# Kernel tuning notes

Measured on AMD Instinct MI355X. Metric: run time of the kernel, lower is better.

Reference implementation:

```python
import jax, jax.numpy as jnp
import numpy as np

HIDDEN_DIM = 2048
N = 4  # expansion_rate
LAYER_IDX = 0
S_ALPHA = 0.01
S_BETA = 0.01
EPS = 1e-5


def setup_inputs() -> dict:
    key = jax.random.key(0)
    k1, k2, k3, k4, k5 = jax.random.split(key, 5)
    batch, seq = 4, 2048
    layer_output = jax.random.normal(k1, (batch, seq, HIDDEN_DIM), dtype=jnp.float32)
    hidden_states = jax.random.normal(k2, (batch, seq, N, HIDDEN_DIM), dtype=jnp.float32)
    # static base matrices (initialization from the torch module)
    B = jnp.ones((1, N), dtype=jnp.float32)
    Am = jnp.zeros((N, 1), dtype=jnp.float32).at[LAYER_IDX % N, 0].set(1.0)
    Ar = jnp.eye(N, dtype=jnp.float32)
    # dynamic parameters
    s_alpha = jnp.full((N, N), S_ALPHA, dtype=jnp.float32)
    s_beta = jnp.full((1, N), S_BETA, dtype=jnp.float32)
    W_beta = jax.random.normal(k3, (HIDDEN_DIM, N), dtype=jnp.float32) * 0.02
    W_m = jax.random.normal(k4, (HIDDEN_DIM, N), dtype=jnp.float32) * 0.02
    W_r = jax.random.normal(k5, (HIDDEN_DIM, N, N), dtype=jnp.float32) * 0.02
    return {
        "layer_output": layer_output,
        "hidden_states": hidden_states,
        "B": B,
        "Am": Am,
        "Ar": Ar,
        "s_alpha": s_alpha,
        "s_beta": s_beta,
        "W_beta": W_beta,
        "W_m": W_m,
        "W_r": W_r,
    }


def reference(layer_output, hidden_states, B, Am, Ar, s_alpha, s_beta, W_beta, W_m, W_r):
    # hidden_states: [b, s, n, d]; layer_output: [b, s, d]
    # --- dynamic matrices ---
    mu = jnp.mean(hidden_states, axis=-1, keepdims=True)
    var = jnp.var(hidden_states, axis=-1, keepdims=True)
    H_norm = (hidden_states - mu) * jax.lax.rsqrt(var + EPS)  # layer_norm, no affine
    H_bar = H_norm.mean(axis=2)  # [b, s, d]

    delta_B = jnp.tanh(H_bar @ W_beta)            # [b, s, n]
    B_dyn = s_beta[0] * delta_B + B[0]            # [b, s, n]
    delta_Am = jnp.tanh(H_bar @ W_m)              # [b, s, n]
    Am_dyn = s_alpha[:, 0] * delta_Am + Am[:, 0]  # [b, s, n]
    delta_Ar = jnp.tanh(jnp.einsum('bsd,dij->bsij', H_bar, W_r))  # [b, s, n, n]
    Ar_dyn = s_alpha * delta_Ar + Ar              # [b, s, n, n]

    # --- combine ---
    depth = B_dyn[..., None] * layer_output[:, :, None, :]                       # [b,s,n,d]
    mixed = jnp.einsum('bsn,bsnd->bsd', Am_dyn, hidden_states)[:, :, None, :]    # [b,s,1,d] broadcasts over n
    residual = jnp.einsum('bsij,bsjd->bsid', Ar_dyn, hidden_states)              # [b,s,n,d]
    return depth + mixed + residual
```

## Files before the change

kernel.cpp:

```cpp
#include <hip/hip_runtime.h>

#define D     2048
#define NEXP  4
#define BLK   256
#define NWAVE 4
#define EPSV  1e-5f

__device__ __forceinline__ unsigned short f2b(float f) {
    union { float f; unsigned int u; } v; v.f = f;
    unsigned int r = (v.u + 0x7fffu + ((v.u >> 16) & 1u)) >> 16;
    return (unsigned short)r;
}
__device__ __forceinline__ float b2f(unsigned short b) {
    union { unsigned int u; float f; } v; v.u = ((unsigned int)b) << 16;
    return v.f;
}

__global__ __launch_bounds__(256) void wt_kernel(
    const float* __restrict__ Wb, const float* __restrict__ Wm,
    const float* __restrict__ Wr, float* __restrict__ Wt)
{
    int idx = blockIdx.x * 256 + threadIdx.x;
    int c = idx / D;
    int d = idx % D;
    float v;
    if (c < 4)       v = Wb[d * 4 + c];
    else if (c < 8)  v = Wm[d * 4 + (c - 4)];
    else             v = Wr[d * 16 + (c - 8)];
    Wt[c * D + d] = v;
}

__global__ __launch_bounds__(BLK) void hc_kernel(
    const float* __restrict__ lo,
    const float* __restrict__ hs,
    const float* __restrict__ Bm,
    const float* __restrict__ Am,
    const float* __restrict__ Ar,
    const float* __restrict__ s_alpha,
    const float* __restrict__ s_beta,
    const float* __restrict__ Wt,
    float* __restrict__ out)
{
    __shared__ unsigned short h16[NEXP][D];
    __shared__ float red[NWAVE][24];
    __shared__ float stats[2][NEXP];
    __shared__ float coef[24];

    const int tid  = threadIdx.x;
    const int wave = tid >> 6;
    const int lane = tid & 63;
    const long tok = blockIdx.x;

    const float4* hs4  = (const float4*)(hs + tok * (long)(NEXP * D));
    const float4* lo4  = (const float4*)(lo + tok * (long)D);
    float4*       out4 = (float4*)(out + tok * (long)(NEXP * D));

    float sum[NEXP], sq[NEXP];
    #pragma unroll
    for (int n = 0; n < NEXP; ++n) { sum[n] = 0.f; sq[n] = 0.f; }

    #pragma unroll
    for (int n = 0; n < NEXP; ++n) {
        #pragma unroll
        for (int k = 0; k < 2; ++k) {
            int d4 = tid + BLK * k;
            float4 v = hs4[n * (D / 4) + d4];
            sum[n] += v.x + v.y + v.z + v.w;
            sq[n]  += v.x * v.x + v.y * v.y + v.z * v.z + v.w * v.w;
            ushort4 p;
            p.x = f2b(v.x); p.y = f2b(v.y); p.z = f2b(v.z); p.w = f2b(v.w);
            ((ushort4*)h16[n])[d4] = p;
        }
    }
    float4 lpre0 = lo4[tid];
    float4 lpre1 = lo4[tid + BLK];

    #pragma unroll
    for (int n = 0; n < NEXP; ++n) {
        #pragma unroll
        for (int off = 32; off > 0; off >>= 1) {
            sum[n] += __shfl_down(sum[n], off, 64);
            sq[n]  += __shfl_down(sq[n],  off, 64);
        }
    }
    if (lane == 0) {
        #pragma unroll
        for (int n = 0; n < NEXP; ++n) {
            red[wave][n]        = sum[n];
            red[wave][NEXP + n] = sq[n];
        }
    }
    __syncthreads();
    if (tid < NEXP) {
        float s = 0.f, s2 = 0.f;
        for (int w = 0; w < NWAVE; ++w) { s += red[w][tid]; s2 += red[w][NEXP + tid]; }
        float m   = s * (1.f / D);
        float var = s2 * (1.f / D) - m * m;
        stats[0][tid] = m;
        stats[1][tid] = rsqrtf(var + EPSV);
    }
    __syncthreads();
    float mu[NEXP], rs[NEXP];
    #pragma unroll
    for (int n = 0; n < NEXP; ++n) { mu[n] = stats[0][n]; rs[n] = stats[1][n]; }

    float acc[24];
    #pragma unroll
    for (int v = 0; v < 24; ++v) acc[v] = 0.f;

    const float4* Wt4 = (const float4*)Wt;

    #pragma unroll
    for (int k = 0; k < 2; ++k) {
        int d4 = tid + BLK * k;
        ushort4 a[NEXP];
        #pragma unroll
        for (int n = 0; n < NEXP; ++n) a[n] = ((const ushort4*)h16[n])[d4];
        float4 hb;
        hb.x = 0.25f * ((b2f(a[0].x) - mu[0]) * rs[0] + (b2f(a[1].x) - mu[1]) * rs[1] +
                        (b2f(a[2].x) - mu[2]) * rs[2] + (b2f(a[3].x) - mu[3]) * rs[3]);
        hb.y = 0.25f * ((b2f(a[0].y) - mu[0]) * rs[0] + (b2f(a[1].y) - mu[1]) * rs[1] +
                        (b2f(a[2].y) - mu[2]) * rs[2] + (b2f(a[3].y) - mu[3]) * rs[3]);
        hb.z = 0.25f * ((b2f(a[0].z) - mu[0]) * rs[0] + (b2f(a[1].z) - mu[1]) * rs[1] +
                        (b2f(a[2].z) - mu[2]) * rs[2] + (b2f(a[3].z) - mu[3]) * rs[3]);
        hb.w = 0.25f * ((b2f(a[0].w) - mu[0]) * rs[0] + (b2f(a[1].w) - mu[1]) * rs[1] +
                        (b2f(a[2].w) - mu[2]) * rs[2] + (b2f(a[3].w) - mu[3]) * rs[3]);
        #pragma unroll
        for (int c = 0; c < 24; ++c) {
            float4 w = Wt4[c * (D / 4) + d4];
            acc[c] += hb.x * w.x + hb.y * w.y + hb.z * w.z + hb.w * w.w;
        }
    }
    #pragma unroll
    for (int v = 0; v < 24; ++v) {
        #pragma unroll
        for (int off = 32; off > 0; off >>= 1)
            acc[v] += __shfl_down(acc[v], off, 64);
    }
    if (lane == 0) {
        #pragma unroll
        for (int v = 0; v < 24; ++v) red[wave][v] = acc[v];
    }
    __syncthreads();
    if (tid < 24) {
        float s = 0.f;
        for (int w = 0; w < NWAVE; ++w) s += red[w][tid];
        float t = tanhf(s);
        float c;
        if (tid < 4) {
            c = s_beta[tid] * t + Bm[tid];
        } else if (tid < 8) {
            int n = tid - 4;
            c = s_alpha[n * 4] * t + Am[n];
        } else {
            int ij = tid - 8;
            c = s_alpha[ij] * t + Ar[ij];
        }
        coef[tid] = c;
    }
    __syncthreads();

    float Bd[NEXP], Amd[NEXP], Ard[NEXP][NEXP];
    #pragma unroll
    for (int n = 0; n < NEXP; ++n) { Bd[n] = coef[n]; Amd[n] = coef[4 + n]; }
    #pragma unroll
    for (int i = 0; i < NEXP; ++i)
        #pragma unroll
        for (int j = 0; j < NEXP; ++j) Ard[i][j] = coef[8 + i * 4 + j];

    #pragma unroll
    for (int k = 0; k < 2; ++k) {
        int d4 = tid + BLK * k;
        float4 h[NEXP];
        #pragma unroll
        for (int n = 0; n < NEXP; ++n) {
            ushort4 a = ((const ushort4*)h16[n])[d4];
            h[n].x = b2f(a.x); h[n].y = b2f(a.y); h[n].z = b2f(a.z); h[n].w = b2f(a.w);
        }
        float4 l = (k == 0) ? lpre0 : lpre1;

        float4 mx = {0.f, 0.f, 0.f, 0.f};
        #pragma unroll
        for (int n = 0; n < NEXP; ++n) {
            mx.x += Amd[n] * h[n].x; mx.y += Amd[n] * h[n].y;
            mx.z += Amd[n] * h[n].z; mx.w += Amd[n] * h[n].w;
        }
        #pragma unroll
        for (int i = 0; i < NEXP; ++i) {
            float4 o;
            o.x = Bd[i] * l.x + mx.x;
            o.y = Bd[i] * l.y + mx.y;
            o.z = Bd[i] * l.z + mx.z;
            o.w = Bd[i] * l.w + mx.w;
            #pragma unroll
            for (int j = 0; j < NEXP; ++j) {
                o.x += Ard[i][j] * h[j].x;
                o.y += Ard[i][j] * h[j].y;
                o.z += Ard[i][j] * h[j].z;
                o.w += Ard[i][j] * h[j].w;
            }
            out4[i * (D / 4) + d4] = o;
        }
    }
}

extern "C" void kernel_launch(void* const* d_in, const int* in_sizes, int n_in,
                              void* d_out, int out_size, void* d_ws, size_t ws_size,
                              hipStream_t stream) {
    const float* lo      = (const float*)d_in[0];
    const float* hs      = (const float*)d_in[1];
    const float* Bm      = (const float*)d_in[2];
    const float* Am      = (const float*)d_in[3];
    const float* Ar      = (const float*)d_in[4];
    const float* s_alpha = (const float*)d_in[5];
    const float* s_beta  = (const float*)d_in[6];
    const float* Wb      = (const float*)d_in[7];
    const float* Wm      = (const float*)d_in[8];
    const float* Wr      = (const float*)d_in[9];
    float* out = (float*)d_out;
    float* Wt  = (float*)d_ws;

    wt_kernel<<<192, 256, 0, stream>>>(Wb, Wm, Wr, Wt);

    const int tokens = in_sizes[0] / D;
    hc_kernel<<<tokens, BLK, 0, stream>>>(lo, hs, Bm, Am, Ar, s_alpha, s_beta,
                                          Wt, out);
}
```

Before: 155.2 us.

## Keep hidden rows in registers and split projection columns across waves

The hidden-state rows are now kept in fp32 registers (32 floats per thread) instead of being packed to bf16 in shared memory. This removes the bf16 conversion, the large LDS footprint, and the bf16 rounding error in the output. H_bar is written to a small LDS buffer, and each wave computes only 6 of the 24 projection columns, so each thread does 6 shuffle reductions instead of 24 and the cross-wave sum goes away. The trade is higher register pressure and an extra barrier, while the total weight-read traffic per block stays the same.

```diff
diff --git a/kernel.cpp b/kernel.cpp
--- a/kernel.cpp
+++ b/kernel.cpp
@@ -5,16 +5,6 @@
 #define BLK   256
 #define NWAVE 4
 #define EPSV  1e-5f
-
-__device__ __forceinline__ unsigned short f2b(float f) {
-    union { float f; unsigned int u; } v; v.f = f;
-    unsigned int r = (v.u + 0x7fffu + ((v.u >> 16) & 1u)) >> 16;
-    return (unsigned short)r;
-}
-__device__ __forceinline__ float b2f(unsigned short b) {
-    union { unsigned int u; float f; } v; v.u = ((unsigned int)b) << 16;
-    return v.f;
-}
 
 __global__ __launch_bounds__(256) void wt_kernel(
     const float* __restrict__ Wb, const float* __restrict__ Wm,
@@ -41,8 +31,8 @@
     const float* __restrict__ Wt,
     float* __restrict__ out)
 {
-    __shared__ unsigned short h16[NEXP][D];
-    __shared__ float red[NWAVE][24];
+    __shared__ float hb_lds[D];
+    __shared__ float red[NWAVE][2 * NEXP];
     __shared__ float stats[2][NEXP];
     __shared__ float coef[24];
 
@@ -55,6 +45,7 @@
     const float4* lo4  = (const float4*)(lo + tok * (long)D);
     float4*       out4 = (float4*)(out + tok * (long)(NEXP * D));
 
+    float4 h[NEXP][2];
     float sum[NEXP], sq[NEXP];
     #pragma unroll
     for (int n = 0; n < NEXP; ++n) { sum[n] = 0.f; sq[n] = 0.f; }
@@ -63,13 +54,10 @@
     for (int n = 0; n < NEXP; ++n) {
         #pragma unroll
         for (int k = 0; k < 2; ++k) {
-            int d4 = tid + BLK * k;
-            float4 v = hs4[n * (D / 4) + d4];
+            float4 v = hs4[n * (D / 4) + tid + BLK * k];
+            h[n][k] = v;
             sum[n] += v.x + v.y + v.z + v.w;
             sq[n]  += v.x * v.x + v.y * v.y + v.z * v.z + v.w * v.w;
-            ushort4 p;
-            p.x = f2b(v.x); p.y = f2b(v.y); p.z = f2b(v.z); p.w = f2b(v.w);
-            ((ushort4*)h16[n])[d4] = p;
         }
     }
     float4 lpre0 = lo4[tid];
@@ -79,8 +67,8 @@
     for (int n = 0; n < NEXP; ++n) {
         #pragma unroll
         for (int off = 32; off > 0; off >>= 1) {
-            sum[n] += __shfl_down(sum[n], off, 64);
-            sq[n]  += __shfl_down(sq[n],  off, 64);
+            sum[n] += __shfl_xor(sum[n], off, 64);
+            sq[n]  += __shfl_xor(sq[n],  off, 64);
         }
     }
     if (lane == 0) {
@@ -93,6 +81,7 @@
     __syncthreads();
     if (tid < NEXP) {
         float s = 0.f, s2 = 0.f;
+        #pragma unroll
         for (int w = 0; w < NWAVE; ++w) { s += red[w][tid]; s2 += red[w][NEXP + tid]; }
         float m   = s * (1.f / D);
         float var = s2 * (1.f / D) - m * m;
@@ -104,48 +93,52 @@
     #pragma unroll
     for (int n = 0; n < NEXP; ++n) { mu[n] = stats[0][n]; rs[n] = stats[1][n]; }
 
-    float acc[24];
-    #pragma unroll
-    for (int v = 0; v < 24; ++v) acc[v] = 0.f;
-
-    const float4* Wt4 = (const float4*)Wt;
-
     #pragma unroll
     for (int k = 0; k < 2; ++k) {
         int d4 = tid + BLK * k;
-        ushort4 a[NEXP];
-        #pragma unroll
-        for (int n = 0; n < NEXP; ++n) a[n] = ((const ushort4*)h16[n])[d4];
         float4 hb;
-        hb.x = 0.25f * ((b2f(a[0].x) - mu[0]) * rs[0] + (b2f(a[1].x) - mu[1]) * rs[1] +
-                        (b2f(a[2].x) - mu[2]) * rs[2] + (b2f(a[3].x) - mu[3]) * rs[3]);
-        hb.y = 0.25f * ((b2f(a[0].y) - mu[0]) * rs[0] + (b2f(a[1].y) - mu[1]) * rs[1] +
-                        (b2f(a[2].y) - mu[2]) * rs[2] + (b2f(a[3].y) - mu[3]) * rs[3]);
-        hb.z = 0.25f * ((b2f(a[0].z) - mu[0]) * rs[0] + (b2f(a[1].z) - mu[1]) * rs[1] +
-                        (b2f(a[2].z) - mu[2]) * rs[2] + (b2f(a[3].z) - mu[3]) * rs[3]);
-        hb.w = 0.25f * ((b2f(a[0].w) - mu[0]) * rs[0] + (b2f(a[1].w) - mu[1]) * rs[1] +
-                        (b2f(a[2].w) - mu[2]) * rs[2] + (b2f(a[3].w) - mu[3]) * rs[3]);
-        #pragma unroll
-        for (int c = 0; c < 24; ++c) {
-            float4 w = Wt4[c * (D / 4) + d4];
+        hb.x = 0.25f * ((h[0][k].x - mu[0]) * rs[0] + (h[1][k].x - mu[1]) * rs[1] +
+                        (h[2][k].x - mu[2]) * rs[2] + (h[3][k].x - mu[3]) * rs[3]);
+        hb.y = 0.25f * ((h[0][k].y - mu[0]) * rs[0] + (h[1][k].y - mu[1]) * rs[1] +
+                        (h[2][k].y - mu[2]) * rs[2] + (h[3][k].y - mu[3]) * rs[3]);
+        hb.z = 0.25f * ((h[0][k].z - mu[0]) * rs[0] + (h[1][k].z - mu[1]) * rs[1] +
+                        (h[2][k].z - mu[2]) * rs[2] + (h[3][k].z - mu[3]) * rs[3]);
+        hb.w = 0.25f * ((h[0][k].w - mu[0]) * rs[0] + (h[1][k].w - mu[1]) * rs[1] +
+                        (h[2][k].w - mu[2]) * rs[2] + (h[3][k].w - mu[3]) * rs[3]);
+        ((float4*)hb_lds)[d4] = hb;
+    }
+    __syncthreads();
+
+    float acc[6];
+    #pragma unroll
+    for (int c = 0; c < 6; ++c) acc[c] = 0.f;
+
+    const int cbase = wave * 6;
+    const float4* Wt4 = (const float4*)Wt;
+
+    #pragma unroll
+    for (int p = 0; p < 8; ++p) {
+        int d4 = p * 64 + lane;
+        float4 hb = ((const float4*)hb_lds)[d4];
+        #pragma unroll
+        for (int c = 0; c < 6; ++c) {
+            float4 w = Wt4[(cbase + c) * (D / 4) + d4];
             acc[c] += hb.x * w.x + hb.y * w.y + hb.z * w.z + hb.w * w.w;
         }
     }
     #pragma unroll
-    for (int v = 0; v < 24; ++v) {
+    for (int c = 0; c < 6; ++c) {
         #pragma unroll
         for (int off = 32; off > 0; off >>= 1)
-            acc[v] += __shfl_down(acc[v], off, 64);
+            acc[c] += __shfl_xor(acc[c], off, 64);
     }
     if (lane == 0) {
         #pragma unroll
-        for (int v = 0; v < 24; ++v) red[wave][v] = acc[v];
+        for (int c = 0; c < 6; ++c) coef[cbase + c] = acc[c];
     }
     __syncthreads();
     if (tid < 24) {
-        float s = 0.f;
-        for (int w = 0; w < NWAVE; ++w) s += red[w][tid];
-        float t = tanhf(s);
+        float t = tanhf(coef[tid]);
         float c;
         if (tid < 4) {
             c = s_beta[tid] * t + Bm[tid];
@@ -171,19 +164,13 @@
     #pragma unroll
     for (int k = 0; k < 2; ++k) {
         int d4 = tid + BLK * k;
-        float4 h[NEXP];
+        float4 l = (k == 0) ? lpre0 : lpre1;
+
+        float4 mx = {0.f, 0.f, 0.f, 0.f};
         #pragma unroll
         for (int n = 0; n < NEXP; ++n) {
-            ushort4 a = ((const ushort4*)h16[n])[d4];
-            h[n].x = b2f(a.x); h[n].y = b2f(a.y); h[n].z = b2f(a.z); h[n].w = b2f(a.w);
-        }
-        float4 l = (k == 0) ? lpre0 : lpre1;
-
-        float4 mx = {0.f, 0.f, 0.f, 0.f};
-        #pragma unroll
-        for (int n = 0; n < NEXP; ++n) {
-            mx.x += Amd[n] * h[n].x; mx.y += Amd[n] * h[n].y;
-            mx.z += Amd[n] * h[n].z; mx.w += Amd[n] * h[n].w;
+            mx.x += Amd[n] * h[n][k].x; mx.y += Amd[n] * h[n][k].y;
+            mx.z += Amd[n] * h[n][k].z; mx.w += Amd[n] * h[n][k].w;
         }
         #pragma unroll
         for (int i = 0; i < NEXP; ++i) {
@@ -194,10 +181,10 @@
             o.w = Bd[i] * l.w + mx.w;
             #pragma unroll
             for (int j = 0; j < NEXP; ++j) {
-                o.x += Ard[i][j] * h[j].x;
-                o.y += Ard[i][j] * h[j].y;
-                o.z += Ard[i][j] * h[j].z;
-                o.w += Ard[i][j] * h[j].w;
+                o.x += Ard[i][j] * h[j][k].x;
+                o.y += Ard[i][j] * h[j][k].y;
+                o.z += Ard[i][j] * h[j][k].z;
+                o.w += Ard[i][j] * h[j][k].w;
             }
             out4[i * (D / 4) + d4] = o;
         }
```

New measurement: 157.2 us. About the same (+1.3%).
